# Performance work log

Hardware: AMD Instinct MI355X
Metric: run time of the kernel (lower is better)

Reference implementation:

```python
import jax, jax.numpy as jnp
import numpy as np

IN_CH = 128
OUT_CH = 128
N_NODES = 50000
N_EDGES = 800000
BN_EPS = 1e-5


def setup_inputs() -> dict:
    key = jax.random.key(0)
    k_x, k_e, k_wl, k_bl, k_wr = jax.random.split(key, 5)
    x = jax.random.normal(k_x, (N_NODES, IN_CH), dtype=jnp.float32)
    edge_index = jax.random.randint(k_e, (2, N_EDGES), 0, N_NODES, dtype=jnp.int64)
    s = 1.0 / np.sqrt(IN_CH)
    W_l = jax.random.uniform(k_wl, (OUT_CH, IN_CH), jnp.float32, -s, s)  # lin_l: aggregated neighbors
    b_l = jax.random.uniform(k_bl, (OUT_CH,), jnp.float32, -s, s)
    W_r = jax.random.uniform(k_wr, (OUT_CH, IN_CH), jnp.float32, -s, s)  # lin_r: root/self
    gamma = jnp.ones((OUT_CH,), jnp.float32)
    beta = jnp.zeros((OUT_CH,), jnp.float32)
    return {"x": x, "edge_index": edge_index, "W_l": W_l, "b_l": b_l,
            "W_r": W_r, "gamma": gamma, "beta": beta}


def reference(x, edge_index, W_l, b_l, W_r, gamma, beta):
    n = x.shape[0]
    src, dst = edge_index[0], edge_index[1]
    # gather source features and mean-aggregate at destination nodes
    msgs = x[src]                                              # [E, C_in]
    agg = jax.ops.segment_sum(msgs, dst, num_segments=n)      # [N, C_in]
    deg = jax.ops.segment_sum(jnp.ones((edge_index.shape[1],), x.dtype), dst, num_segments=n)
    mean_agg = agg / jnp.maximum(deg, 1.0)[:, None]
    # SAGEConv: lin_l(aggregated) + lin_r(self)
    h = mean_agg @ W_l.T + b_l + x @ W_r.T                     # [N, C_out]
    # BatchNorm1d (training-mode batch statistics, biased variance)
    mu = h.mean(axis=0)
    var = ((h - mu) ** 2).mean(axis=0)
    h = (h - mu) * jax.lax.rsqrt(var + BN_EPS) * gamma + beta
    return jax.nn.relu(h)
```

## Files before the change

kernel.cpp:

```cpp
#include <hip/hip_runtime.h>

#define CH 128
#define BN_EPS 1e-5f

typedef unsigned int uint32;
typedef unsigned short ushort16;
using f32x2  = __attribute__((ext_vector_type(2))) float;
using f32x4  = __attribute__((ext_vector_type(4))) float;
using bf16x8 = __attribute__((ext_vector_type(8))) short;

__device__ __forceinline__ ushort16 f2b(float f) {
    uint32 u = __float_as_uint(f);
    return (ushort16)((u + 0x7FFFu + ((u >> 16) & 1u)) >> 16);
}
__device__ __forceinline__ uint32 pk2(float a, float b) {
    return (uint32)f2b(a) | ((uint32)f2b(b) << 16);
}
__device__ __forceinline__ float blo(uint32 u) { return __uint_as_float(u << 16); }
__device__ __forceinline__ float bhi(uint32 u) { return __uint_as_float(u & 0xFFFF0000u); }

__global__ __launch_bounds__(256) void sage_prep(
    const float* __restrict__ x, const void* __restrict__ ei,
    const float* __restrict__ Wl, const float* __restrict__ Wr,
    int* __restrict__ head, int2* __restrict__ pair,
    uint32* __restrict__ xb4, uint2* __restrict__ xq8,
    ushort16* __restrict__ wct, float* __restrict__ bn,
    int nEdges, int total8)
{
    const int* pi = (const int*)ei;
    int lane = threadIdx.x & 63;
    int probe = pi[lane * 2 + 1];
    bool is64 = (__ballot(probe != 0) == 0ULL);

    int idx = blockIdx.x * 256 + threadIdx.x;

    const float4* x4 = (const float4*)x;
    float4 a = make_float4(0, 0, 0, 0), b = make_float4(0, 0, 0, 0);
    bool hasC = (idx < total8);
    if (hasC) { a = x4[2 * idx]; b = x4[2 * idx + 1]; }

    if (idx < nEdges) {
        int s, d;
        if (is64) {
            const long long* p = (const long long*)ei;
            s = (int)p[idx];
            d = (int)p[nEdges + idx];
        } else {
            s = pi[idx];
            d = pi[nEdges + idx];
        }
        int old = atomicExch(&head[d], idx);
        pair[idx] = make_int2(old, s);
    }

    if (hasC) {
        uint4 o;
        o.x = pk2(a.x, a.y); o.y = pk2(a.z, a.w);
        o.z = pk2(b.x, b.y); o.w = pk2(b.z, b.w);
        ((uint4*)xb4)[idx] = o;

        int qa = __builtin_amdgcn_cvt_pk_fp8_f32(a.x, a.y, 0, false);
        qa = __builtin_amdgcn_cvt_pk_fp8_f32(a.z, a.w, qa, true);
        int qb = __builtin_amdgcn_cvt_pk_fp8_f32(b.x, b.y, 0, false);
        qb = __builtin_amdgcn_cvt_pk_fp8_f32(b.z, b.w, qb, true);
        xq8[idx] = make_uint2((uint32)qa, (uint32)qb);
    }

    if (blockIdx.x < 128) {
        int widx = blockIdx.x * 256 + threadIdx.x;
        int co = widx >> 8, k = widx & 255;
        float v = (k < 128) ? Wr[co * 128 + k] : Wl[co * 128 + (k - 128)];
        wct[widx] = f2b(v);
    }
    if (blockIdx.x == 0) bn[threadIdx.x] = 0.f;
    if (blockIdx.x == 1 && threadIdx.x < 32)
        ((uint32*)(xq8))[(size_t)total8 * 2 + threadIdx.x] = 0;
}

__global__ __launch_bounds__(256) void sage_aggregate(
    const char* __restrict__ xq, const int* __restrict__ head,
    const int2* __restrict__ pair, uint32* __restrict__ mean_b, int nNodes)
{
    int wid = blockIdx.x * 4 + (threadIdx.x >> 6);
    int nbase = wid * 8;
    if (nbase >= nNodes) return;
    int lane = threadIdx.x & 63;
    int chain = lane >> 3;
    int sub = lane & 7;

    const int ZROW = nNodes;

    int cur = -1;
    if (lane < 8) {
        int n = nbase + lane;
        cur = (n < nNodes) ? head[n] : -1;
    }
    int cnt = 0;
    f32x2 acc2[8];
    #pragma unroll
    for (int i = 0; i < 8; ++i) acc2[i] = (f32x2){0.f, 0.f};

    while (__ballot(cur >= 0) != 0ULL) {
        int2 pr = make_int2(-1, ZROW);
        if (cur >= 0) pr = pair[cur];
        int s = __shfl(pr.y, chain);
        uint4 u = *(const uint4*)(xq + ((size_t)s << 7) + sub * 16);
        #pragma unroll
        for (int w = 0; w < 4; ++w) {
            uint32 uw = (&u.x)[w];
            acc2[w * 2 + 0] += __builtin_amdgcn_cvt_pk_f32_fp8((int)uw, false);
            acc2[w * 2 + 1] += __builtin_amdgcn_cvt_pk_f32_fp8((int)uw, true);
        }
        if (cur >= 0) { ++cnt; cur = pr.x; }
    }

    int cn = __shfl(cnt, chain);
    float inv = 1.0f / fmaxf((float)cn, 1.0f);
    int n = nbase + chain;
    if (n < nNodes) {
        uint4 o0 = make_uint4(pk2(acc2[0][0] * inv, acc2[0][1] * inv),
                              pk2(acc2[1][0] * inv, acc2[1][1] * inv),
                              pk2(acc2[2][0] * inv, acc2[2][1] * inv),
                              pk2(acc2[3][0] * inv, acc2[3][1] * inv));
        uint4 o1 = make_uint4(pk2(acc2[4][0] * inv, acc2[4][1] * inv),
                              pk2(acc2[5][0] * inv, acc2[5][1] * inv),
                              pk2(acc2[6][0] * inv, acc2[6][1] * inv),
                              pk2(acc2[7][0] * inv, acc2[7][1] * inv));
        char* base = (char*)mean_b + (size_t)n * 256 + sub * 32;
        *(uint4*)base = o0;
        *(uint4*)(base + 16) = o1;
    }
}

__global__ __launch_bounds__(256) void sage_gemm(
    const ushort16* __restrict__ xb, const ushort16* __restrict__ mean_b,
    const ushort16* __restrict__ wct, const float* __restrict__ bl,
    ushort16* __restrict__ hb, float* __restrict__ bn, int nNodes)
{
    __shared__ ushort16 wsh[8 * 8 * 64 * 8];
    __shared__ float redS[4][CH];
    __shared__ float redQ[4][CH];

    int tid = threadIdx.x;
    int wave = tid >> 6, lane = tid & 63;
    int col = lane & 15, kg = lane >> 4;

    #pragma unroll
    for (int it = 0; it < 16; ++it) {
        int pidx = wave * 16 + it;
        int cb = pidx >> 3, ks = pidx & 7;
        bf16x8 v = *(const bf16x8*)(wct + (size_t)(cb * 16 + col) * 256 + ks * 32 + kg * 8);
        *(bf16x8*)(wsh + ((size_t)pidx * 64 + lane) * 8) = v;
    }

    int rowBase = blockIdx.x * 64 + wave * 16;
    int arow = min(rowBase + col, nNodes - 1);
    const ushort16* xrow = xb + (size_t)arow * CH;
    const ushort16* mrow = mean_b + (size_t)arow * CH;

    bf16x8 afrag[8];
    #pragma unroll
    for (int t = 0; t < 4; ++t)
        afrag[t] = *(const bf16x8*)(xrow + t * 32 + kg * 8);
    #pragma unroll
    for (int t = 0; t < 4; ++t)
        afrag[4 + t] = *(const bf16x8*)(mrow + t * 32 + kg * 8);

    __syncthreads();

    f32x4 acc[8];
    #pragma unroll
    for (int cb = 0; cb < 8; ++cb) acc[cb] = (f32x4){0.f, 0.f, 0.f, 0.f};

    #pragma unroll
    for (int kstep = 0; kstep < 8; ++kstep) {
        bf16x8 a = afrag[kstep];
        #pragma unroll
        for (int cb = 0; cb < 8; ++cb) {
            bf16x8 b = *(const bf16x8*)(wsh + ((size_t)(cb * 8 + kstep) * 64 + lane) * 8);
            acc[cb] = __builtin_amdgcn_mfma_f32_16x16x32_bf16(a, b, acc[cb], 0, 0, 0);
        }
    }

    #pragma unroll
    for (int cb = 0; cb < 8; ++cb) {
        int co = cb * 16 + col;
        float blv = bl[co];
        float s = 0.f, ss = 0.f;
        #pragma unroll
        for (int j = 0; j < 4; ++j) {
            int r = rowBase + kg * 4 + j;
            float v = acc[cb][j] + blv;
            if (r < nNodes) {
                hb[(size_t)r * CH + co] = f2b(v);
                s += v;
                ss += v * v;
            }
        }
        s  += __shfl_xor(s, 16);  s  += __shfl_xor(s, 32);
        ss += __shfl_xor(ss, 16); ss += __shfl_xor(ss, 32);
        if (kg == 0) { redS[wave][co] = s; redQ[wave][co] = ss; }
    }
    __syncthreads();
    if (tid < CH) {
        atomicAdd(&bn[tid], redS[0][tid] + redS[1][tid] + redS[2][tid] + redS[3][tid]);
    } else {
        int c = tid - CH;
        atomicAdd(&bn[CH + c], redQ[0][c] + redQ[1][c] + redQ[2][c] + redQ[3][c]);
    }
}

__global__ __launch_bounds__(256) void sage_apply(
    const ushort16* __restrict__ hb, float* __restrict__ out,
    const float* __restrict__ bn, const float* __restrict__ gamma,
    const float* __restrict__ beta, int total8, int nNodes)
{
    __shared__ float sc_sh[CH], sh_sh[CH];
    int tid = threadIdx.x;
    if (tid < CH) {
        float invN = 1.0f / (float)nNodes;
        float mu = bn[tid] * invN;
        float var = fmaxf(bn[CH + tid] * invN - mu * mu, 0.f);
        float sc = gamma[tid] * rsqrtf(var + BN_EPS);
        sc_sh[tid] = sc;
        sh_sh[tid] = beta[tid] - mu * sc;
    }
    __syncthreads();
    int i = blockIdx.x * 256 + tid;
    if (i >= total8) return;
    uint4 u = *(const uint4*)(hb + (size_t)i * 8);
    int c = (i * 8) & 127;
    float4 o0, o1;
    o0.x = fmaxf(fmaf(blo(u.x), sc_sh[c + 0], sh_sh[c + 0]), 0.f);
    o0.y = fmaxf(fmaf(bhi(u.x), sc_sh[c + 1], sh_sh[c + 1]), 0.f);
    o0.z = fmaxf(fmaf(blo(u.y), sc_sh[c + 2], sh_sh[c + 2]), 0.f);
    o0.w = fmaxf(fmaf(bhi(u.y), sc_sh[c + 3], sh_sh[c + 3]), 0.f);
    o1.x = fmaxf(fmaf(blo(u.z), sc_sh[c + 4], sh_sh[c + 4]), 0.f);
    o1.y = fmaxf(fmaf(bhi(u.z), sc_sh[c + 5], sh_sh[c + 5]), 0.f);
    o1.z = fmaxf(fmaf(blo(u.w), sc_sh[c + 6], sh_sh[c + 6]), 0.f);
    o1.w = fmaxf(fmaf(bhi(u.w), sc_sh[c + 7], sh_sh[c + 7]), 0.f);
    float4* dst = (float4*)(out + (size_t)i * 8);
    dst[0] = o0;
    dst[1] = o1;
}

extern "C" void kernel_launch(void* const* d_in, const int* in_sizes, int n_in,
                              void* d_out, int out_size, void* d_ws, size_t ws_size,
                              hipStream_t stream)
{
    const float* x     = (const float*)d_in[0];
    const void*  ei    = d_in[1];
    const float* Wl    = (const float*)d_in[2];
    const float* bl    = (const float*)d_in[3];
    const float* Wr    = (const float*)d_in[4];
    const float* gamma = (const float*)d_in[5];
    const float* beta  = (const float*)d_in[6];

    int nNodes = in_sizes[0] / CH;
    int nEdges = in_sizes[1] / 2;
    int nBlkM  = (nNodes + 63) / 64;

    char* p = (char*)d_ws;
    auto take = [&](size_t bytes) {
        char* r = p;
        p += (bytes + 255) & ~(size_t)255;
        return r;
    };
    ushort16* xb      = (ushort16*)take((size_t)nNodes * CH * 2);
    char*     xq      = (char*)take((size_t)nNodes * CH + 128);
    ushort16* mean_b  = (ushort16*)take((size_t)nNodes * CH * 2);
    ushort16* hb      = (ushort16*)take((size_t)nNodes * CH * 2);
    ushort16* wct     = (ushort16*)take((size_t)CH * 256 * 2);
    int*      head    = (int*)take((size_t)nNodes * 4);
    float*    bn      = (float*)take(256 * 4);
    int2*     pair    = (int2*)take((size_t)nEdges * 8);

    float* out = (float*)d_out;

    hipMemsetAsync(head, 0xFF, (size_t)nNodes * 4, stream);

    int total8 = nNodes * CH / 8;
    int eBlocks = (nEdges + 255) / 256;
    int pBlocks = max(eBlocks, (total8 + 255) / 256);
    sage_prep<<<pBlocks, 256, 0, stream>>>(
        x, ei, Wl, Wr, head, pair, (uint32*)xb, (uint2*)xq, wct, bn,
        nEdges, total8);

    int aBlocks = (nNodes + 31) / 32;
    sage_aggregate<<<aBlocks, 256, 0, stream>>>(
        xq, head, pair, (uint32*)mean_b, nNodes);

    sage_gemm<<<nBlkM, 256, 0, stream>>>(
        xb, mean_b, wct, bl, hb, bn, nNodes);

    sage_apply<<<(total8 + 255) / 256, 256, 0, stream>>>(
        hb, out, bn, gamma, beta, total8, nNodes);
}
```

Baseline: 124.6 us.

## Prefetch next edge pair in aggregation, double GEMM rows per block, kernel head init

The aggregation loop now loads the next linked-list pair before processing the current one, so the dependent pointer-chasing load overlaps with the feature gather. The GEMM kernel handles 128 rows per block with two accumulator sets, which reuses each LDS weight fragment twice and halves the block count. The memset of the head array is replaced by a small init kernel. Together these raise register pressure and cut the number of GEMM blocks, which may lower occupancy.

```diff
diff --git a/kernel.cpp b/kernel.cpp
--- a/kernel.cpp
+++ b/kernel.cpp
@@ -25,7 +25,7 @@
     int* __restrict__ head, int2* __restrict__ pair,
     uint32* __restrict__ xb4, uint2* __restrict__ xq8,
     ushort16* __restrict__ wct, float* __restrict__ bn,
-    int nEdges, int total8)
+    int nEdges, int nNodes, int total8)
 {
     const int* pi = (const int*)ei;
     int lane = threadIdx.x & 63;
@@ -77,6 +77,11 @@
         ((uint32*)(xq8))[(size_t)total8 * 2 + threadIdx.x] = 0;
 }
 
+__global__ __launch_bounds__(256) void sage_init(int* __restrict__ head, int nNodes) {
+    int i = blockIdx.x * 256 + threadIdx.x;
+    if (i < nNodes) head[i] = -1;
+}
+
 __global__ __launch_bounds__(256) void sage_aggregate(
     const char* __restrict__ xq, const int* __restrict__ head,
     const int2* __restrict__ pair, uint32* __restrict__ mean_b, int nNodes)
@@ -100,9 +105,14 @@
     #pragma unroll
     for (int i = 0; i < 8; ++i) acc2[i] = (f32x2){0.f, 0.f};
 
+    int2 pr = make_int2(-1, ZROW);
+    if (cur >= 0) pr = pair[cur];
+
     while (__ballot(cur >= 0) != 0ULL) {
-        int2 pr = make_int2(-1, ZROW);
-        if (cur >= 0) pr = pair[cur];
+        int nxt = pr.x;
+        int2 prn = make_int2(-1, ZROW);
+        if (cur >= 0 && nxt >= 0) prn = pair[nxt];
+
         int s = __shfl(pr.y, chain);
         uint4 u = *(const uint4*)(xq + ((size_t)s << 7) + sub * 16);
         #pragma unroll
@@ -111,7 +121,8 @@
             acc2[w * 2 + 0] += __builtin_amdgcn_cvt_pk_f32_fp8((int)uw, false);
             acc2[w * 2 + 1] += __builtin_amdgcn_cvt_pk_f32_fp8((int)uw, true);
         }
-        if (cur >= 0) { ++cnt; cur = pr.x; }
+        if (cur >= 0) { ++cnt; cur = nxt; }
+        pr = prn;
     }
 
     int cn = __shfl(cnt, chain);
@@ -153,32 +164,40 @@
         *(bf16x8*)(wsh + ((size_t)pidx * 64 + lane) * 8) = v;
     }
 
-    int rowBase = blockIdx.x * 64 + wave * 16;
-    int arow = min(rowBase + col, nNodes - 1);
-    const ushort16* xrow = xb + (size_t)arow * CH;
-    const ushort16* mrow = mean_b + (size_t)arow * CH;
-
-    bf16x8 afrag[8];
-    #pragma unroll
-    for (int t = 0; t < 4; ++t)
-        afrag[t] = *(const bf16x8*)(xrow + t * 32 + kg * 8);
-    #pragma unroll
-    for (int t = 0; t < 4; ++t)
-        afrag[4 + t] = *(const bf16x8*)(mrow + t * 32 + kg * 8);
+    int row0 = blockIdx.x * 128 + wave * 16;
+    int row1 = row0 + 64;
+    int arow0 = min(row0 + col, nNodes - 1);
+    int arow1 = min(row1 + col, nNodes - 1);
+    const ushort16* xr0 = xb + (size_t)arow0 * CH;
+    const ushort16* mr0 = mean_b + (size_t)arow0 * CH;
+    const ushort16* xr1 = xb + (size_t)arow1 * CH;
+    const ushort16* mr1 = mean_b + (size_t)arow1 * CH;
+
+    bf16x8 af0[8], af1[8];
+    #pragma unroll
+    for (int t = 0; t < 4; ++t) {
+        af0[t]     = *(const bf16x8*)(xr0 + t * 32 + kg * 8);
+        af0[4 + t] = *(const bf16x8*)(mr0 + t * 32 + kg * 8);
+        af1[t]     = *(const bf16x8*)(xr1 + t * 32 + kg * 8);
+        af1[4 + t] = *(const bf16x8*)(mr1 + t * 32 + kg * 8);
+    }
 
     __syncthreads();
 
-    f32x4 acc[8];
-    #pragma unroll
-    for (int cb = 0; cb < 8; ++cb) acc[cb] = (f32x4){0.f, 0.f, 0.f, 0.f};
+    f32x4 acc0[8], acc1[8];
+    #pragma unroll
+    for (int cb = 0; cb < 8; ++cb) {
+        acc0[cb] = (f32x4){0.f, 0.f, 0.f, 0.f};
+        acc1[cb] = (f32x4){0.f, 0.f, 0.f, 0.f};
+    }
 
     #pragma unroll
     for (int kstep = 0; kstep < 8; ++kstep) {
-        bf16x8 a = afrag[kstep];
         #pragma unroll
         for (int cb = 0; cb < 8; ++cb) {
             bf16x8 b = *(const bf16x8*)(wsh + ((size_t)(cb * 8 + kstep) * 64 + lane) * 8);
-            acc[cb] = __builtin_amdgcn_mfma_f32_16x16x32_bf16(a, b, acc[cb], 0, 0, 0);
+            acc0[cb] = __builtin_amdgcn_mfma_f32_16x16x32_bf16(af0[kstep], b, acc0[cb], 0, 0, 0);
+            acc1[cb] = __builtin_amdgcn_mfma_f32_16x16x32_bf16(af1[kstep], b, acc1[cb], 0, 0, 0);
         }
     }
 
@@ -189,12 +208,17 @@
         float s = 0.f, ss = 0.f;
         #pragma unroll
         for (int j = 0; j < 4; ++j) {
-            int r = rowBase + kg * 4 + j;
-            float v = acc[cb][j] + blv;
-            if (r < nNodes) {
-                hb[(size_t)r * CH + co] = f2b(v);
-                s += v;
-                ss += v * v;
+            int r0 = row0 + kg * 4 + j;
+            float v0 = acc0[cb][j] + blv;
+            if (r0 < nNodes) {
+                hb[(size_t)r0 * CH + co] = f2b(v0);
+                s += v0; ss += v0 * v0;
+            }
+            int r1 = row1 + kg * 4 + j;
+            float v1 = acc1[cb][j] + blv;
+            if (r1 < nNodes) {
+                hb[(size_t)r1 * CH + co] = f2b(v1);
+                s += v1; ss += v1 * v1;
             }
         }
         s  += __shfl_xor(s, 16);  s  += __shfl_xor(s, 32);
@@ -258,7 +282,7 @@
 
     int nNodes = in_sizes[0] / CH;
     int nEdges = in_sizes[1] / 2;
-    int nBlkM  = (nNodes + 63) / 64;
+    int nBlkM  = (nNodes + 127) / 128;
 
     char* p = (char*)d_ws;
     auto take = [&](size_t bytes) {
@@ -277,14 +301,15 @@
 
     float* out = (float*)d_out;
 
-    hipMemsetAsync(head, 0xFF, (size_t)nNodes * 4, stream);
-
     int total8 = nNodes * CH / 8;
     int eBlocks = (nEdges + 255) / 256;
     int pBlocks = max(eBlocks, (total8 + 255) / 256);
+
+    sage_init<<<(nNodes + 255) / 256, 256, 0, stream>>>(head, nNodes);
+
     sage_prep<<<pBlocks, 256, 0, stream>>>(
         x, ei, Wl, Wr, head, pair, (uint32*)xb, (uint2*)xq, wct, bn,
-        nEdges, total8);
+        nEdges, nNodes, total8);
 
     int aBlocks = (nNodes + 31) / 32;
     sage_aggregate<<<aBlocks, 256, 0, stream>>>(
```

Result: faster. 115.9 us (-7.0%).
